# Kernel tuning notes

Hardware: AMD Instinct MI355X
Metric: run time of the kernel (lower is better)

The kernel has to match this reference:

```python
import jax, jax.numpy as jnp
import numpy as np

B, S, D, F, E, TOP_K = 4, 2048, 1024, 4096, 8, 2


def setup_inputs() -> dict:
    key = jax.random.key(0)
    ks = jax.random.split(key, 6)
    sd = 1.0 / np.sqrt(D)
    sf = 1.0 / np.sqrt(F)
    return {
        "x": jax.random.normal(ks[0], (B, S, D), dtype=jnp.float32),
        "router_w": jax.random.normal(ks[1], (E, D), dtype=jnp.float32) * sd,
        "router_b": jnp.zeros((E,), dtype=jnp.float32),
        "w1": jax.random.normal(ks[2], (E, F, D), dtype=jnp.float32) * sd,  # Linear(d_model->d_ff) weight [out,in]
        "w2": jax.random.normal(ks[3], (E, D, F), dtype=jnp.float32) * sf,  # Linear(d_ff->d_model)
        "w3": jax.random.normal(ks[4], (E, F, D), dtype=jnp.float32) * sd,
    }


def reference(x, router_w, router_b, w1, w2, w3):
    # Router: softmax over experts, then top-k with renormalized gates.
    logits = jnp.einsum("bsd,ed->bse", x, router_w) + router_b          # [B,S,E]
    probs = jax.nn.softmax(logits, axis=-1)
    topk_p, topk_i = jax.lax.top_k(probs, TOP_K)                         # [B,S,K]
    topk_p = topk_p / jnp.sum(topk_p, axis=-1, keepdims=True)
    # Per-token combine weight for each expert (0 if not selected).
    combine = jnp.sum(jax.nn.one_hot(topk_i, E, dtype=x.dtype) * topk_p[..., None], axis=-2)  # [B,S,E]

    # Note: expert(x*mask)*mask == expert(x)*mask since SwiGLU(0)=0 (no bias).
    out = jnp.zeros_like(x)
    for e in range(E):  # small fixed expert count
        h = jax.nn.silu(jnp.einsum("bsd,fd->bsf", x, w1[e])) * jnp.einsum("bsd,fd->bsf", x, w3[e])
        out = out + combine[..., e:e + 1] * jnp.einsum("bsf,df->bsd", h, w2[e])
    return out
```

## Files before the change

### kernel.cpp

```cpp
#include <hip/hip_runtime.h>
#include <hip/hip_fp16.h>


#define NTOK 8192
#define D_ 1024
#define F_ 4096
#define E_ 8
#define SLOT_CAP 18432

using half8 = __attribute__((ext_vector_type(8))) _Float16;
using half4 = __attribute__((ext_vector_type(4))) _Float16;
using f32x4 = __attribute__((ext_vector_type(4))) float;

__device__ __forceinline__ void gload16(const void* g, void* l) {
  __builtin_amdgcn_global_load_lds((const __attribute__((address_space(1))) void*)g,
                                   (__attribute__((address_space(3))) void*)l, 16, 0, 0);
}

__global__ __launch_bounds__(256) void cvt_kernel(const float* __restrict__ src,
                                                  _Float16* __restrict__ dst, int n4) {
  int i = blockIdx.x * 256 + threadIdx.x;
  int stride = gridDim.x * 256;
  for (; i < n4; i += stride) {
    float4 v = ((const float4*)src)[i];
    half4 h;
    h.x = (_Float16)v.x; h.y = (_Float16)v.y; h.z = (_Float16)v.z; h.w = (_Float16)v.w;
    ((half4*)dst)[i] = h;
  }
}

__global__ __launch_bounds__(256) void cvt_w13_kernel(const float* __restrict__ w1,
                                                      const float* __restrict__ w3,
                                                      _Float16* __restrict__ w13, int n4) {
  int i = blockIdx.x * 256 + threadIdx.x;
  int stride = gridDim.x * 256;
  for (; i < n4; i += stride) {
    int d4 = i & 255;
    int row = i >> 8;
    int e = row >> 12, f = row & 4095;
    size_t vbase = ((size_t)e << 13) | ((size_t)(f >> 4) << 5) | (size_t)(f & 15);
    float4 v1 = ((const float4*)w1)[i];
    float4 v3 = ((const float4*)w3)[i];
    half4 h1, h3;
    h1.x = (_Float16)v1.x; h1.y = (_Float16)v1.y; h1.z = (_Float16)v1.z; h1.w = (_Float16)v1.w;
    h3.x = (_Float16)v3.x; h3.y = (_Float16)v3.y; h3.z = (_Float16)v3.z; h3.w = (_Float16)v3.w;
    ((half4*)w13)[vbase * 256 + d4] = h1;
    ((half4*)w13)[(vbase + 16) * 256 + d4] = h3;
  }
}

__global__ __launch_bounds__(256) void router_kernel(
    const float* __restrict__ x, const float* __restrict__ rw, const float* __restrict__ rbias,
    _Float16* __restrict__ x16, int* __restrict__ tok_e, float* __restrict__ tok_g,
    int* __restrict__ counts) {
  int wv = threadIdx.x >> 6, lane = threadIdx.x & 63;
  int t = blockIdx.x * 4 + wv;
  const float4* xr = (const float4*)(x + (size_t)t * D_);
  float acc[E_];
#pragma unroll
  for (int e = 0; e < E_; ++e) acc[e] = 0.f;
  for (int i = lane; i < D_ / 4; i += 64) {
    float4 xv = xr[i];
    half4 hx;
    hx.x = (_Float16)xv.x; hx.y = (_Float16)xv.y; hx.z = (_Float16)xv.z; hx.w = (_Float16)xv.w;
    ((half4*)(x16 + (size_t)t * D_))[i] = hx;
#pragma unroll
    for (int e = 0; e < E_; ++e) {
      float4 wv4 = ((const float4*)(rw + (size_t)e * D_))[i];
      acc[e] += xv.x * wv4.x + xv.y * wv4.y + xv.z * wv4.z + xv.w * wv4.w;
    }
  }
#pragma unroll
  for (int e = 0; e < E_; ++e) {
#pragma unroll
    for (int off = 32; off > 0; off >>= 1) acc[e] += __shfl_down(acc[e], off);
  }
  if (lane == 0) {
    float p[E_], mx = -1e30f;
#pragma unroll
    for (int e = 0; e < E_; ++e) { p[e] = acc[e] + rbias[e]; mx = fmaxf(mx, p[e]); }
#pragma unroll
    for (int e = 0; e < E_; ++e) p[e] = expf(p[e] - mx);
    int i0 = 0;
#pragma unroll
    for (int e = 1; e < E_; ++e) if (p[e] > p[i0]) i0 = e;
    int i1 = (i0 == 0) ? 1 : 0;
#pragma unroll
    for (int e = 0; e < E_; ++e) if (e != i0 && p[e] > p[i1]) i1 = e;
    float s = p[i0] + p[i1];
    tok_e[t * 2] = i0; tok_e[t * 2 + 1] = i1;
    tok_g[t * 2] = p[i0] / s; tok_g[t * 2 + 1] = p[i1] / s;
    atomicAdd(&counts[i0], 1); atomicAdd(&counts[i1], 1);
  }
}

__global__ void init_kernel(int* slot_token, int* counts, int* cursor) {
  int i = blockIdx.x * 256 + threadIdx.x;
  if (blockIdx.x == 0 && threadIdx.x < E_) { counts[threadIdx.x] = 0; cursor[threadIdx.x] = 0; }
  if (i < SLOT_CAP) slot_token[i] = 0;
}

__global__ void scan_kernel(const int* __restrict__ counts, int* __restrict__ offs) {
  if (threadIdx.x == 0) {
    int o = 0;
    for (int e = 0; e < E_; ++e) { offs[e] = o; o += ((counts[e] + 255) / 256) * 256; }
    offs[E_] = o;
  }
}

__global__ void scatter_kernel(const int* __restrict__ tok_e, const int* __restrict__ offs,
                               int* __restrict__ cursor, int* __restrict__ slot_token,
                               int* __restrict__ slot_of) {
  int i = blockIdx.x * 256 + threadIdx.x;
  if (i >= NTOK * 2) return;
  int e = tok_e[i];
  int pos = offs[e] + atomicAdd(&cursor[e], 1);
  slot_token[pos] = i >> 1;
  slot_of[i] = pos;
}

template <int MODE, int ORD, int KD, int NBN, int RPX, int BEROWS>
__global__ __launch_bounds__(512, 2) void moe_gemm_kernel(
    const _Float16* __restrict__ Amat, const _Float16* __restrict__ Bmat,
    const int* __restrict__ slot_token, const int* __restrict__ offs,
    void* __restrict__ outp) {
  constexpr int BM = 256;
  constexpr int MROW = 8;
  constexpr int AINS = 2;
  constexpr int S = AINS + 2;
  constexpr int AH = BM * 32;
  constexpr int BUFH = (BM + 256) * 32;
  constexpr int NT = KD / 32;
  __shared__ _Float16 lds[4 * BUFH];

  int id = blockIdx.x;
  int xcd = id & 7, idx = id >> 3;
  int rb, nb;
  if constexpr (ORD == 0) {
    int band = idx / (8 * NBN);
    int i2 = idx - band * (8 * NBN);
    int rib = (RPX - band * 8) < 8 ? (RPX - band * 8) : 8;
    nb = i2 / rib;
    rb = xcd * RPX + band * 8 + (i2 - nb * rib);
  } else {
    nb = idx % NBN;
    rb = xcd * RPX + idx / NBN;
  }
  int row0 = rb * BM;
  if (row0 >= offs[E_]) return;
  int e = 0;
#pragma unroll
  for (int i = 1; i < E_; ++i) if (row0 >= offs[i]) e = i;

  int t = threadIdx.x, l = t & 63, w = t >> 6;
  int wr = w >> 2, wc = w & 3;
  int srow = t >> 2;
  int gsrc8 = ((l & 3) ^ ((l >> 3) & 3)) * 8;

  const _Float16* aP[AINS];
  if constexpr (MODE == 0) {
#pragma unroll
    for (int ins = 0; ins < AINS; ++ins) {
      int tk = slot_token[row0 + srow + ins * 128];
      aP[ins] = Amat + (size_t)tk * KD + gsrc8;
    }
  } else {
#pragma unroll
    for (int ins = 0; ins < AINS; ++ins)
      aP[ins] = Amat + (size_t)(row0 + srow + ins * 128) * KD + gsrc8;
  }
  const _Float16* b0P = Bmat + ((size_t)e * BEROWS + (size_t)nb * 256 + srow) * KD + gsrc8;
  const _Float16* b1P = b0P + (size_t)128 * KD;

  int fr = l & 15, kg = l >> 4;
  int swz8 = (kg ^ ((fr >> 1) & 3)) * 8;
  const int rA = (wr * 128 + fr) * 32 + swz8;
  const int rB = AH + (wc * 64 + fr) * 32 + swz8;

  f32x4 acc[MROW][4];
#pragma unroll
  for (int m = 0; m < MROW; ++m)
#pragma unroll
    for (int n = 0; n < 4; ++n) acc[m][n] = (f32x4){0.f, 0.f, 0.f, 0.f};

#pragma unroll
  for (int ins = 0; ins < AINS; ++ins) gload16(aP[ins], &lds[ins * 4096 + w * 512]);
  gload16(b0P, &lds[AH + w * 512]);
  gload16(b1P, &lds[AH + 4096 + w * 512]);
#pragma unroll
  for (int ins = 0; ins < AINS; ++ins) gload16(aP[ins] + 32, &lds[BUFH + ins * 4096 + w * 512]);
  gload16(b0P + 32, &lds[BUFH + AH + w * 512]);
  gload16(b1P + 32, &lds[BUFH + AH + 4096 + w * 512]);
  asm volatile("s_waitcnt vmcnt(%0)" ::"i"(S) : "memory");
  __builtin_amdgcn_s_barrier();
  __builtin_amdgcn_sched_barrier(0);

#pragma unroll
  for (int ins = 0; ins < AINS; ++ins) aP[ins] += 64;
  b0P += 64; b1P += 64;

#define GEMM_STEP(U, PRE2, WN)                                                        \
  {                                                                                   \
    constexpr int bi_ = (U) & 3;                                                      \
    constexpr int bs_ = ((U) + 2) & 3;                                                \
    if (PRE2) {                                                                       \
      _Pragma("unroll") for (int ins = 0; ins < AINS; ++ins)                          \
          gload16(aP[ins] + (U) * 32, &lds[bs_ * BUFH + ins * 4096 + w * 512]);       \
      gload16(b0P + (U) * 32, &lds[bs_ * BUFH + AH + w * 512]);                       \
      gload16(b1P + (U) * 32, &lds[bs_ * BUFH + AH + 4096 + w * 512]);                \
    }                                                                                 \
    half8 a_[MROW], b_[4];                                                            \
    _Pragma("unroll") for (int mi = 0; mi < MROW; ++mi)                               \
        a_[mi] = *(const half8*)&lds[bi_ * BUFH + rA + mi * 512];                     \
    _Pragma("unroll") for (int ni = 0; ni < 4; ++ni)                                  \
        b_[ni] = *(const half8*)&lds[bi_ * BUFH + rB + ni * 512];                     \
    __builtin_amdgcn_s_setprio(1);                                                    \
    _Pragma("unroll") for (int mi = 0; mi < MROW; ++mi)                               \
        _Pragma("unroll") for (int ni = 0; ni < 4; ++ni)                              \
            acc[mi][ni] = __builtin_amdgcn_mfma_f32_16x16x32_f16(a_[mi], b_[ni],      \
                                                                 acc[mi][ni], 0, 0, 0); \
    __builtin_amdgcn_s_setprio(0);                                                    \
    if ((WN) >= 0) {                                                                  \
      asm volatile("s_waitcnt vmcnt(%0)" ::"i"((WN) >= 0 ? (WN) : 0) : "memory");     \
      __builtin_amdgcn_s_barrier();                                                   \
      __builtin_amdgcn_sched_barrier(0);                                              \
    }                                                                                 \
  }

  for (int j4 = 0; j4 < NT - 4; j4 += 4) {
    GEMM_STEP(0, true, S)
    GEMM_STEP(1, true, S)
    GEMM_STEP(2, true, S)
    GEMM_STEP(3, true, S)
#pragma unroll
    for (int ins = 0; ins < AINS; ++ins) aP[ins] += 128;
    b0P += 128; b1P += 128;
  }
  GEMM_STEP(0, true, S)
  GEMM_STEP(1, true, S)
  GEMM_STEP(2, false, 0)
  GEMM_STEP(3, false, -1)
#undef GEMM_STEP

  int q4 = kg * 4;
  if constexpr (MODE == 0) {
    _Float16* hb = (_Float16*)outp;
#pragma unroll
    for (int mi = 0; mi < MROW; ++mi) {
      size_t rbase = (size_t)(row0 + wr * 128 + mi * 16 + q4);
#pragma unroll
      for (int p = 0; p < 2; ++p) {
        int fc = nb * 128 + (wc * 2 + p) * 16 + fr;
#pragma unroll
        for (int i = 0; i < 4; ++i) {
          float gv = acc[mi][2 * p][i];
          float hv = gv / (1.f + __expf(-gv)) * acc[mi][2 * p + 1][i];
          hb[(rbase + i) * (size_t)F_ + fc] = (_Float16)hv;
        }
      }
    }
  } else {
    float* yb = (float*)outp;
#pragma unroll
    for (int mi = 0; mi < MROW; ++mi) {
      size_t rbase = (size_t)(row0 + wr * 128 + mi * 16 + q4);
#pragma unroll
      for (int ni = 0; ni < 4; ++ni) {
        int col = nb * 256 + wc * 64 + ni * 16 + fr;
#pragma unroll
        for (int i = 0; i < 4; ++i)
          yb[(rbase + i) * (size_t)D_ + col] = acc[mi][ni][i];
      }
    }
  }
}

__global__ __launch_bounds__(256) void combine_kernel(
    const float* __restrict__ ybuf, const int* __restrict__ slot_of,
    const float* __restrict__ tok_g, float* __restrict__ out) {
  int t = blockIdx.x, i = threadIdx.x;
  int s0 = slot_of[t * 2], s1 = slot_of[t * 2 + 1];
  float g0 = tok_g[t * 2], g1 = tok_g[t * 2 + 1];
  float4 a = ((const float4*)(ybuf + (size_t)s0 * D_))[i];
  float4 b = ((const float4*)(ybuf + (size_t)s1 * D_))[i];
  float4 r;
  r.x = g0 * a.x + g1 * b.x;
  r.y = g0 * a.y + g1 * b.y;
  r.z = g0 * a.z + g1 * b.z;
  r.w = g0 * a.w + g1 * b.w;
  ((float4*)(out + (size_t)t * D_))[i] = r;
}

extern "C" void kernel_launch(void* const* d_in, const int* in_sizes, int n_in,
                              void* d_out, int out_size, void* d_ws, size_t ws_size,
                              hipStream_t stream) {
  const float* x  = (const float*)d_in[0];
  const float* rw = (const float*)d_in[1];
  const float* rbc = (const float*)d_in[2];
  const float* w1 = (const float*)d_in[3];
  const float* w2 = (const float*)d_in[4];
  const float* w3 = (const float*)d_in[5];
  float* out = (float*)d_out;

  char* ws = (char*)d_ws;
  size_t off = 0;
  auto take = [&](size_t bytes) {
    char* p = ws + off;
    off = (off + bytes + 255) & ~(size_t)255;
    return p;
  };
  _Float16* x16 = (_Float16*)take((size_t)NTOK * D_ * 2);
  _Float16* w13 = (_Float16*)take((size_t)E_ * 2 * F_ * D_ * 2);
  _Float16* w2h = (_Float16*)take((size_t)E_ * D_ * F_ * 2);
  _Float16* hbuf = (_Float16*)take((size_t)SLOT_CAP * F_ * 2);
  float* ybuf = (float*)take((size_t)SLOT_CAP * D_ * 4);
  int* slot_token = (int*)take((size_t)SLOT_CAP * 4);
  int* tok_e = (int*)take((size_t)NTOK * 2 * 4);
  float* tok_g = (float*)take((size_t)NTOK * 2 * 4);
  int* slot_of = (int*)take((size_t)NTOK * 2 * 4);
  int* counts = (int*)take(E_ * 4);
  int* cursor = (int*)take(E_ * 4);
  int* offs = (int*)take((E_ + 1) * 4);

  cvt_w13_kernel<<<4096, 256, 0, stream>>>(w1, w3, w13, E_ * F_ * D_ / 4);
  cvt_kernel<<<4096, 256, 0, stream>>>(w2, w2h, E_ * D_ * F_ / 4);
  init_kernel<<<(SLOT_CAP + 255) / 256, 256, 0, stream>>>(slot_token, counts, cursor);
  router_kernel<<<NTOK / 4, 256, 0, stream>>>(x, rw, rbc, x16, tok_e, tok_g, counts);
  scan_kernel<<<1, 64, 0, stream>>>(counts, offs);
  scatter_kernel<<<(NTOK * 2 + 255) / 256, 256, 0, stream>>>(tok_e, offs, cursor, slot_token, slot_of);
  moe_gemm_kernel<0, 0, 1024, 32, 9, 8192><<<2304, 512, 0, stream>>>(
      x16, w13, slot_token, offs, (void*)hbuf);
  moe_gemm_kernel<1, 1, 4096, 4, 9, 1024><<<288, 512, 0, stream>>>(
      hbuf, w2h, slot_token, offs, (void*)ybuf);
  combine_kernel<<<NTOK, 256, 0, stream>>>(ybuf, slot_of, tok_g, out);
}
```

Measured before the change: 917.2 us.

## Software-pipeline LDS fragment loads with MFMAs and deepen global prefetch

```diff
diff --git a/kernel.cpp b/kernel.cpp
--- a/kernel.cpp
+++ b/kernel.cpp
@@ -126,8 +126,6 @@
     void* __restrict__ outp) {
   constexpr int BM = 256;
   constexpr int MROW = 8;
-  constexpr int AINS = 2;
-  constexpr int S = AINS + 2;
   constexpr int AH = BM * 32;
   constexpr int BUFH = (BM + 256) * 32;
   constexpr int NT = KD / 32;
@@ -157,17 +155,16 @@
   int srow = t >> 2;
   int gsrc8 = ((l & 3) ^ ((l >> 3) & 3)) * 8;
 
-  const _Float16* aP[AINS];
+  const _Float16* aP0;
+  const _Float16* aP1;
   if constexpr (MODE == 0) {
-#pragma unroll
-    for (int ins = 0; ins < AINS; ++ins) {
-      int tk = slot_token[row0 + srow + ins * 128];
-      aP[ins] = Amat + (size_t)tk * KD + gsrc8;
-    }
+    int tk0 = slot_token[row0 + srow];
+    int tk1 = slot_token[row0 + srow + 128];
+    aP0 = Amat + (size_t)tk0 * KD + gsrc8;
+    aP1 = Amat + (size_t)tk1 * KD + gsrc8;
   } else {
-#pragma unroll
-    for (int ins = 0; ins < AINS; ++ins)
-      aP[ins] = Amat + (size_t)(row0 + srow + ins * 128) * KD + gsrc8;
+    aP0 = Amat + (size_t)(row0 + srow) * KD + gsrc8;
+    aP1 = Amat + (size_t)(row0 + srow + 128) * KD + gsrc8;
   }
   const _Float16* b0P = Bmat + ((size_t)e * BEROWS + (size_t)nb * 256 + srow) * KD + gsrc8;
   const _Float16* b1P = b0P + (size_t)128 * KD;
@@ -177,6 +174,8 @@
   const int rA = (wr * 128 + fr) * 32 + swz8;
   const int rB = AH + (wc * 64 + fr) * 32 + swz8;
 
+  half8 aF[MROW];
+  half8 bF[4];
   f32x4 acc[MROW][4];
 #pragma unroll
   for (int m = 0; m < MROW; ++m)
@@ -184,63 +183,79 @@
     for (int n = 0; n < 4; ++n) acc[m][n] = (f32x4){0.f, 0.f, 0.f, 0.f};
 
 #pragma unroll
-  for (int ins = 0; ins < AINS; ++ins) gload16(aP[ins], &lds[ins * 4096 + w * 512]);
-  gload16(b0P, &lds[AH + w * 512]);
-  gload16(b1P, &lds[AH + 4096 + w * 512]);
-#pragma unroll
-  for (int ins = 0; ins < AINS; ++ins) gload16(aP[ins] + 32, &lds[BUFH + ins * 4096 + w * 512]);
-  gload16(b0P + 32, &lds[BUFH + AH + w * 512]);
-  gload16(b1P + 32, &lds[BUFH + AH + 4096 + w * 512]);
-  asm volatile("s_waitcnt vmcnt(%0)" ::"i"(S) : "memory");
+  for (int tt = 0; tt < 3; ++tt) {
+    gload16(aP0 + tt * 32, &lds[tt * BUFH + w * 512]);
+    gload16(aP1 + tt * 32, &lds[tt * BUFH + 4096 + w * 512]);
+    gload16(b0P + tt * 32, &lds[tt * BUFH + AH + w * 512]);
+    gload16(b1P + tt * 32, &lds[tt * BUFH + AH + 4096 + w * 512]);
+  }
+  asm volatile("s_waitcnt vmcnt(4)" ::: "memory");
   __builtin_amdgcn_s_barrier();
   __builtin_amdgcn_sched_barrier(0);
-
-#pragma unroll
-  for (int ins = 0; ins < AINS; ++ins) aP[ins] += 64;
-  b0P += 64; b1P += 64;
-
-#define GEMM_STEP(U, PRE2, WN)                                                        \
-  {                                                                                   \
-    constexpr int bi_ = (U) & 3;                                                      \
-    constexpr int bs_ = ((U) + 2) & 3;                                                \
-    if (PRE2) {                                                                       \
-      _Pragma("unroll") for (int ins = 0; ins < AINS; ++ins)                          \
-          gload16(aP[ins] + (U) * 32, &lds[bs_ * BUFH + ins * 4096 + w * 512]);       \
-      gload16(b0P + (U) * 32, &lds[bs_ * BUFH + AH + w * 512]);                       \
-      gload16(b1P + (U) * 32, &lds[bs_ * BUFH + AH + 4096 + w * 512]);                \
-    }                                                                                 \
-    half8 a_[MROW], b_[4];                                                            \
-    _Pragma("unroll") for (int mi = 0; mi < MROW; ++mi)                               \
-        a_[mi] = *(const half8*)&lds[bi_ * BUFH + rA + mi * 512];                     \
-    _Pragma("unroll") for (int ni = 0; ni < 4; ++ni)                                  \
-        b_[ni] = *(const half8*)&lds[bi_ * BUFH + rB + ni * 512];                     \
-    __builtin_amdgcn_s_setprio(1);                                                    \
-    _Pragma("unroll") for (int mi = 0; mi < MROW; ++mi)                               \
-        _Pragma("unroll") for (int ni = 0; ni < 4; ++ni)                              \
-            acc[mi][ni] = __builtin_amdgcn_mfma_f32_16x16x32_f16(a_[mi], b_[ni],      \
-                                                                 acc[mi][ni], 0, 0, 0); \
-    __builtin_amdgcn_s_setprio(0);                                                    \
-    if ((WN) >= 0) {                                                                  \
-      asm volatile("s_waitcnt vmcnt(%0)" ::"i"((WN) >= 0 ? (WN) : 0) : "memory");     \
-      __builtin_amdgcn_s_barrier();                                                   \
-      __builtin_amdgcn_sched_barrier(0);                                              \
-    }                                                                                 \
+#pragma unroll
+  for (int m = 0; m < MROW; ++m) aF[m] = *(const half8*)&lds[rA + m * 512];
+#pragma unroll
+  for (int n = 0; n < 4; ++n) bF[n] = *(const half8*)&lds[rB + n * 512];
+  __builtin_amdgcn_sched_barrier(0);
+  aP0 += 96; aP1 += 96; b0P += 96; b1P += 96;
+
+#define MF4_(mm)                                                                         \
+  acc[mm][0] = __builtin_amdgcn_mfma_f32_16x16x32_f16(aF[mm], bF[0], acc[mm][0], 0, 0, 0); \
+  acc[mm][1] = __builtin_amdgcn_mfma_f32_16x16x32_f16(aF[mm], bF[1], acc[mm][1], 0, 0, 0); \
+  acc[mm][2] = __builtin_amdgcn_mfma_f32_16x16x32_f16(aF[mm], bF[2], acc[mm][2], 0, 0, 0); \
+  acc[mm][3] = __builtin_amdgcn_mfma_f32_16x16x32_f16(aF[mm], bF[3], acc[mm][3], 0, 0, 0);
+
+#define GSTEP(U, PRE, WN)                                                     \
+  {                                                                           \
+    constexpr int bn_ = ((U) + 1) & 3;                                        \
+    constexpr int bs_ = ((U) + 3) & 3;                                        \
+    if (PRE) {                                                                \
+      gload16(aP0 + (U) * 32, &lds[bs_ * BUFH + w * 512]);                    \
+      gload16(aP1 + (U) * 32, &lds[bs_ * BUFH + 4096 + w * 512]);             \
+      gload16(b0P + (U) * 32, &lds[bs_ * BUFH + AH + w * 512]);               \
+      gload16(b1P + (U) * 32, &lds[bs_ * BUFH + AH + 4096 + w * 512]);        \
+    }                                                                         \
+    const _Float16* nb_ = &lds[bn_ * BUFH];                                   \
+    asm volatile("s_waitcnt lgkmcnt(0)" ::: "memory");                        \
+    __builtin_amdgcn_sched_barrier(0);                                        \
+    __builtin_amdgcn_s_setprio(1);                                            \
+    MF4_(0) aF[0] = *(const half8*)(nb_ + rA);                                \
+    MF4_(1) aF[1] = *(const half8*)(nb_ + rA + 512);                          \
+    MF4_(2) aF[2] = *(const half8*)(nb_ + rA + 1024);                         \
+    MF4_(3) aF[3] = *(const half8*)(nb_ + rA + 1536);                         \
+    MF4_(4) aF[4] = *(const half8*)(nb_ + rA + 2048);                         \
+    MF4_(5) aF[5] = *(const half8*)(nb_ + rA + 2560);                         \
+    MF4_(6) aF[6] = *(const half8*)(nb_ + rA + 3072);                         \
+    MF4_(7) aF[7] = *(const half8*)(nb_ + rA + 3584);                         \
+    bF[0] = *(const half8*)(nb_ + rB);                                        \
+    bF[1] = *(const half8*)(nb_ + rB + 512);                                  \
+    bF[2] = *(const half8*)(nb_ + rB + 1024);                                 \
+    bF[3] = *(const half8*)(nb_ + rB + 1536);                                 \
+    __builtin_amdgcn_s_setprio(0);                                            \
+    if ((WN) >= 0) {                                                          \
+      asm volatile("s_waitcnt vmcnt(%0)" ::"i"((WN) >= 0 ? (WN) : 0) : "memory"); \
+      __builtin_amdgcn_s_barrier();                                           \
+      __builtin_amdgcn_sched_barrier(0);                                      \
+    }                                                                         \
   }
 
   for (int j4 = 0; j4 < NT - 4; j4 += 4) {
-    GEMM_STEP(0, true, S)
-    GEMM_STEP(1, true, S)
-    GEMM_STEP(2, true, S)
-    GEMM_STEP(3, true, S)
-#pragma unroll
-    for (int ins = 0; ins < AINS; ++ins) aP[ins] += 128;
-    b0P += 128; b1P += 128;
-  }
-  GEMM_STEP(0, true, S)
-  GEMM_STEP(1, true, S)
-  GEMM_STEP(2, false, 0)
-  GEMM_STEP(3, false, -1)
-#undef GEMM_STEP
+    GSTEP(0, true, 4)
+    GSTEP(1, true, 4)
+    GSTEP(2, true, 4)
+    GSTEP(3, true, 4)
+    aP0 += 128; aP1 += 128; b0P += 128; b1P += 128;
+  }
+  GSTEP(0, true, 4)
+  GSTEP(1, false, 0)
+  GSTEP(2, false, -1)
+  asm volatile("s_waitcnt lgkmcnt(0)" ::: "memory");
+  __builtin_amdgcn_sched_barrier(0);
+  __builtin_amdgcn_s_setprio(1);
+  MF4_(0) MF4_(1) MF4_(2) MF4_(3) MF4_(4) MF4_(5) MF4_(6) MF4_(7)
+  __builtin_amdgcn_s_setprio(0);
+#undef GSTEP
+#undef MF4_
 
   int q4 = kg * 4;
   if constexpr (MODE == 0) {
```

Measured after the change: 912.5 us. No clear change (-0.5%).
